# Performance work log

Measured on AMD Instinct MI355X. Metric: run time of the kernel, lower is better.

Reference implementation:

```python
import jax, jax.numpy as jnp
import numpy as np

EPS = 1e-5
SLOPE = 0.01  # torch LeakyReLU default negative slope


def _bn(h, gamma, beta):
    # BatchNorm1d in training mode: biased batch statistics over the batch dim
    mu = jnp.mean(h, axis=0)
    var = jnp.var(h, axis=0)
    return gamma * (h - mu) * jax.lax.rsqrt(var + EPS) + beta


def _leaky(h):
    return jnp.where(h >= 0, h, SLOPE * h)


def _forward(x, adj, w_gc1, b_gc1, w_gc2, b_gc2, w_gc3, b_gc3,
             w_fc0, b_fc0, g_fc0, be_fc0, w_fc1, b_fc1, g_fc1, be_fc1, w_fc2, b_fc2):
    B, S, Fp1 = x.shape
    F = Fp1 - 1
    N = adj.shape[0]
    # --- scatter: build per-sample node features from first S-1 timesteps ---
    sids = x[:, :S - 1, -2].astype(jnp.int32)                                   # [B,S-1]
    feats = jnp.concatenate([x[:, :S - 1, :-2], x[:, :S - 1, -1:]], axis=-1)    # [B,S-1,F]
    X = jnp.zeros((B, N, F), x.dtype).at[jnp.arange(B)[:, None], sids].set(feats)
    # --- symmetric-normalized adjacency with self loops: D^-1/2 (A+I) D^-1/2 ---
    A = adj + jnp.eye(N, dtype=adj.dtype)
    d = jax.lax.rsqrt(jnp.sum(A, axis=1))
    Ahat = d[:, None] * A * d[None, :]                                          # [N,N]
    # --- fc0 branch on last-timestep features ---
    h0 = _leaky(_bn(x[:, -1, :-2] @ w_fc0 + b_fc0, g_fc0, be_fc0))              # [B,FH]
    # --- 3-layer GCN: relu(Ahat @ X @ W + b) ---
    X = jax.nn.relu(jnp.einsum('mn,bnf->bmf', Ahat, X) @ w_gc1 + b_gc1)
    X = jax.nn.relu(jnp.einsum('mn,bnf->bmf', Ahat, X) @ w_gc2 + b_gc2)
    X = jax.nn.relu(jnp.einsum('mn,bnf->bmf', Ahat, X) @ w_gc3 + b_gc3)         # [B,N,GH]
    # --- gather station-specific rows ---
    sid_last = x[:, -1, -2].astype(jnp.int32)                                   # [B]
    g = X[jnp.arange(B), sid_last]                                              # [B,GH]
    # --- fusion MLP head ---
    h = jnp.concatenate([h0, g], axis=1)
    h = _leaky(_bn(h @ w_fc1 + b_fc1, g_fc1, be_fc1))
    return jax.nn.sigmoid(h @ w_fc2 + b_fc2)                                    # [B,1]


def setup_inputs() -> dict:
    B, N, S, F = 128, 2000, 64, 16
    GH, FH = 512, 512
    key = jax.random.key(0)
    ks = jax.random.split(key, 12)
    x = jax.random.normal(ks[0], (B, S, F + 1), dtype=jnp.float32)
    # station-id column (-2): unique ids per sample so scatter writes are unambiguous
    perms = jax.vmap(lambda k: jax.random.permutation(k, N)[:S])(jax.random.split(ks[1], B))  # [B,S]
    x = x.at[:, :, -2].set(perms.astype(jnp.float32))
    # random symmetric 0/1 adjacency, avg degree ~32
    adj = (jax.random.uniform(ks[2], (N, N)) < (32.0 / N)).astype(jnp.float32)
    adj = jnp.maximum(adj, adj.T)

    def lin(k, i, o):
        kw, kb = jax.random.split(k)
        bound = 1.0 / np.sqrt(i)
        w = jax.random.uniform(kw, (i, o), jnp.float32, -bound, bound)
        b = jax.random.uniform(kb, (o,), jnp.float32, -bound, bound)
        return w, b

    w_gc1, b_gc1 = lin(ks[3], F, GH // 2)
    w_gc2, b_gc2 = lin(ks[4], GH // 2, GH // 2)
    w_gc3, b_gc3 = lin(ks[5], GH // 2, GH)
    w_fc0, b_fc0 = lin(ks[6], F - 1, FH)
    w_fc1, b_fc1 = lin(ks[7], GH + FH, FH)
    w_fc2, b_fc2 = lin(ks[8], FH, 1)
    g_fc0 = jnp.ones((FH,), jnp.float32)
    be_fc0 = jnp.zeros((FH,), jnp.float32)
    g_fc1 = jnp.ones((FH,), jnp.float32)
    be_fc1 = jnp.zeros((FH,), jnp.float32)
    return dict(x=x, adj=adj, w_gc1=w_gc1, b_gc1=b_gc1, w_gc2=w_gc2, b_gc2=b_gc2,
                w_gc3=w_gc3, b_gc3=b_gc3, w_fc0=w_fc0, b_fc0=b_fc0, g_fc0=g_fc0, be_fc0=be_fc0,
                w_fc1=w_fc1, b_fc1=b_fc1, g_fc1=g_fc1, be_fc1=be_fc1, w_fc2=w_fc2, b_fc2=b_fc2)


def reference(x, adj, w_gc1, b_gc1, w_gc2, b_gc2, w_gc3, b_gc3, w_fc0, b_fc0, g_fc0, be_fc0,
              w_fc1, b_fc1, g_fc1, be_fc1, w_fc2, b_fc2):
    return _forward(x, adj, w_gc1, b_gc1, w_gc2, b_gc2, w_gc3, b_gc3,
                    w_fc0, b_fc0, g_fc0, be_fc0, w_fc1, b_fc1, g_fc1, be_fc1, w_fc2, b_fc2)
```

## Files before the change

### kernel.cpp

```cpp
#include <hip/hip_runtime.h>
#include <hip/hip_bf16.h>

typedef __hip_bfloat16 bf16;
typedef short s8v __attribute__((ext_vector_type(8)));
typedef float f4v __attribute__((ext_vector_type(4)));
typedef float f2v __attribute__((ext_vector_type(2)));

#define B   128
#define N   2000
#define S   64
#define CAP 128
#define JT  16
#define JG  8
#define XROW 1088

__device__ inline ushort bfb(float v) {
    union { __hip_bfloat16 h; ushort u; } c; c.h = __float2bfloat16(v); return c.u;
}

__global__ __launch_bounds__(256) void k_prep0(const float* __restrict__ adj,
                                               float* __restrict__ d,
                                               const float* __restrict__ w1,
                                               const float* __restrict__ w2,
                                               uint4* __restrict__ wf1,
                                               uint4* __restrict__ wf2) {
    int blk = blockIdx.x;
    if (blk < N) {
        int m = blk;
        const float* row = adj + (size_t)m * N;
        float s = 0.f;
        for (int c = threadIdx.x; c < N; c += 256) s += row[c];
        for (int o = 32; o > 0; o >>= 1) s += __shfl_down(s, o);
        __shared__ float red[4];
        int wave = threadIdx.x >> 6;
        if ((threadIdx.x & 63) == 0) red[wave] = s;
        __syncthreads();
        if (threadIdx.x == 0)
            d[m] = rsqrtf(red[0] + red[1] + red[2] + red[3] + 1.0f);
    } else {
        int blk2 = blk - N;
        if (blk2 < 4) {
            int e = blk2 * 256 + threadIdx.x;
            int ct = e >> 6, l = e & 63;
            int kg = l >> 4, ch = ct * 16 + (l & 15);
            ushort h[8];
#pragma unroll
            for (int j = 0; j < 8; ++j) {
                int f = kg * 8 + j;
                h[j] = (f < 16) ? bfb(w1[f * 256 + ch]) : (ushort)0;
            }
            uint4 r;
            r.x = h[0] | ((uint)h[1] << 16);
            r.y = h[2] | ((uint)h[3] << 16);
            r.z = h[4] | ((uint)h[5] << 16);
            r.w = h[6] | ((uint)h[7] << 16);
            wf1[e] = r;
        } else {
            int e = (blk2 - 4) * 256 + threadIdx.x;
            int l = e & 63;
            int kc = (e >> 6) & 7;
            int nt = e >> 9;
            int col = l & 15, kg = l >> 4;
            ushort h[8];
#pragma unroll
            for (int i = 0; i < 8; ++i) {
                int k = kc * 32 + kg * 8 + i;
                h[i] = bfb(w2[k * 256 + nt * 16 + col]);
            }
            uint4 r;
            r.x = h[0] | ((uint)h[1] << 16);
            r.y = h[2] | ((uint)h[3] << 16);
            r.z = h[4] | ((uint)h[5] << 16);
            r.w = h[6] | ((uint)h[7] << 16);
            wf2[e] = r;
        }
    }
}

__global__ __launch_bounds__(256) void k_prep1(const float* __restrict__ adj,
                                               const float* __restrict__ d,
                                               const float* __restrict__ x,
                                               int* __restrict__ cnt,
                                               int* __restrict__ idx,
                                               float* __restrict__ val,
                                               int* __restrict__ sid,
                                               int* __restrict__ sid_last,
                                               uint4* __restrict__ feA,
                                               const float* __restrict__ w0,
                                               const float* __restrict__ b0,
                                               float* __restrict__ hp0,
                                               float* __restrict__ mu0,
                                               float* __restrict__ rstd0) {
    int blk = blockIdx.x;
    if (blk < 500) {
        int m = blk * 4 + (threadIdx.x >> 6);
        int lane = threadIdx.x & 63;
        const float* row = adj + (size_t)m * N;
        float dm = d[m];
        int base = 0;
        for (int c0 = 0; c0 < N; c0 += 64) {
            int c = c0 + lane;
            float a = 0.f;
            if (c < N) { a = row[c]; if (c == m) a += 1.0f; }
            bool pred = (a != 0.f);
            unsigned long long mask = __ballot(pred);
            int pos = base + __popcll(mask & ((1ull << lane) - 1ull));
            if (pred && pos < CAP) {
                idx[m * CAP + pos] = c;
                val[m * CAP + pos] = dm * d[c] * a;
            }
            base += (int)__popcll(mask);
        }
        if (lane == 0) cnt[m] = base < CAP ? base : CAP;
    } else if (blk < 500 + B) {
        int b = blk - 500, tid = threadIdx.x;
        const float* xb = x + (size_t)b * XROW;
        __shared__ float dss_sh[63];
        __shared__ float fe_sh[64][16];
        if (tid < S - 1) {
            int s_ = (int)xb[tid * 17 + 15];
            sid[b * (S - 1) + tid] = s_;
            dss_sh[tid] = d[s_];
        }
        if (tid == S - 1) sid_last[b] = (int)xb[(S - 1) * 17 + 15];
        if (tid >= 240 && tid < 256) fe_sh[63][tid - 240] = 0.f;
        __syncthreads();
        for (int i = tid; i < (S - 1) * 16; i += 256) {
            int t = i >> 4, f = i & 15;
            fe_sh[t][f] = dss_sh[t] * xb[t * 17 + (f < 15 ? f : 16)];
        }
        __syncthreads();
        if (tid < 128) {
            int kc = tid >> 6, l = tid & 63;
            int f = l & 15, tg = l >> 4;
            ushort h[8];
#pragma unroll
            for (int j = 0; j < 8; ++j)
                h[j] = bfb(fe_sh[kc * 32 + tg * 8 + j][f]);
            uint4 r;
            r.x = h[0] | ((uint)h[1] << 16);
            r.y = h[2] | ((uint)h[3] << 16);
            r.z = h[4] | ((uint)h[5] << 16);
            r.w = h[6] | ((uint)h[7] << 16);
            feA[(b * 2 + kc) * 64 + l] = r;
        }
    } else {
        int tid = threadIdx.x;
        int c = tid >> 7, b = tid & 127;
        int o = (blk - 500 - B) * 2 + c;
        const float* xr = x + (size_t)b * XROW + (S - 1) * 17;
        float acc = b0[o];
#pragma unroll
        for (int f = 0; f < 15; ++f) acc += xr[f] * w0[f * 512 + o];
        hp0[b * 512 + o] = acc;
        float s = acc, s2 = acc * acc;
        for (int off = 32; off > 0; off >>= 1) {
            s += __shfl_down(s, off);
            s2 += __shfl_down(s2, off);
        }
        __shared__ float rs[4], rs2[4];
        int wv = tid >> 6;
        if ((tid & 63) == 0) { rs[wv] = s; rs2[wv] = s2; }
        __syncthreads();
        if ((tid & 127) == 0) {
            float S1 = rs[c * 2] + rs[c * 2 + 1];
            float S2 = rs2[c * 2] + rs2[c * 2 + 1];
            float m = S1 * (1.f / B);
            float var = S2 * (1.f / B) - m * m;
            mu0[o] = m;
            rstd0[o] = rsqrtf(var + 1e-5f);
        }
    }
}

__global__ __launch_bounds__(256) void k_x1(const float* __restrict__ adj,
                                            const float* __restrict__ d,
                                            const int* __restrict__ sid,
                                            const uint4* __restrict__ feA,
                                            const uint4* __restrict__ wfrag,
                                            const float* __restrict__ b1,
                                            unsigned char* __restrict__ X1) {
    __shared__ int sv[64];
    __shared__ float b1s[256];
    __shared__ __align__(16) union SU {
        ushort Ylds[64][40];
        uint   Xs[4][16][68];
    } su;
    int b = blockIdx.y, p0 = blockIdx.x * 64, tid = threadIdx.x;
    b1s[tid] = b1[tid];
    if (tid < 63) sv[tid] = sid[b * 63 + tid];
    if (tid == 63) sv[63] = 0;
    __syncthreads();

    int l = tid & 63, wv = tid >> 6;
    int lm = l & 15, lg = l >> 4;
    int pt = p0 + wv * 16;
    int pcol = pt + lm;
    bool pv = (pcol < N);
    int pc = pv ? pcol : 0;

    s8v a1_0 = *(const s8v*)&feA[(b * 2 + 0) * 64 + l];
    s8v a1_1 = *(const s8v*)&feA[(b * 2 + 1) * 64 + l];

    int ss[16];
#pragma unroll
    for (int q = 0; q < 16; ++q)
        ss[q] = sv[(q >> 3) * 32 + lg * 8 + (q & 7)];
    float av[16];
#pragma unroll
    for (int q = 0; q < 16; ++q)
        av[q] = adj[(size_t)ss[q] * N + pc];
#pragma unroll
    for (int q = 0; q < 16; ++q) {
        av[q] = pv ? av[q] : 0.f;
        if (pcol == ss[q]) av[q] += 1.0f;
    }
    ushort h[16];
#pragma unroll
    for (int q = 0; q < 16; ++q) h[q] = bfb(av[q]);
    s8v b1f, b2f;
    {
        uint4 t0, t1;
        t0.x = h[0] | ((uint)h[1] << 16);  t0.y = h[2] | ((uint)h[3] << 16);
        t0.z = h[4] | ((uint)h[5] << 16);  t0.w = h[6] | ((uint)h[7] << 16);
        t1.x = h[8] | ((uint)h[9] << 16);  t1.y = h[10] | ((uint)h[11] << 16);
        t1.z = h[12] | ((uint)h[13] << 16); t1.w = h[14] | ((uint)h[15] << 16);
        b1f = *(s8v*)&t0; b2f = *(s8v*)&t1;
    }
    f4v D1 = (f4v){0.f, 0.f, 0.f, 0.f};
    D1 = __builtin_amdgcn_mfma_f32_16x16x32_bf16(a1_0, b1f, D1, 0, 0, 0);
    D1 = __builtin_amdgcn_mfma_f32_16x16x32_bf16(a1_1, b2f, D1, 0, 0, 0);
    float dp = d[pc] * (pv ? 1.f : 0.f);
    uint2 pk;
    pk.x = bfb(D1[0] * dp) | ((uint)bfb(D1[1] * dp) << 16);
    pk.y = bfb(D1[2] * dp) | ((uint)bfb(D1[3] * dp) << 16);
    *(uint2*)&su.Ylds[wv * 16 + lm][lg * 4] = pk;
    *(uint2*)&su.Ylds[wv * 16 + lm][16 + lg * 4] = make_uint2(0u, 0u);
    __syncthreads();

    s8v yf = *(const s8v*)&su.Ylds[wv * 16 + lm][lg * 8];
    __syncthreads();
    f4v acc2[16];
#pragma unroll
    for (int ct = 0; ct < 16; ++ct) acc2[ct] = (f4v){0.f, 0.f, 0.f, 0.f};
#pragma unroll
    for (int ct = 0; ct < 16; ++ct) {
        s8v wfv = *(const s8v*)&wfrag[ct * 64 + l];
        acc2[ct] = __builtin_amdgcn_mfma_f32_16x16x32_bf16(wfv, yf, acc2[ct], 0, 0, 0);
    }
#pragma unroll
    for (int ct = 0; ct < 16; ++ct) {
        float4 bz = *(float4*)&b1s[ct * 16 + lg * 4];
        float v0 = acc2[ct][0] + bz.x; v0 = v0 > 0.f ? v0 : 0.f;
        float v1 = acc2[ct][1] + bz.y; v1 = v1 > 0.f ? v1 : 0.f;
        float v2 = acc2[ct][2] + bz.z; v2 = v2 > 0.f ? v2 : 0.f;
        float v3 = acc2[ct][3] + bz.w; v3 = v3 > 0.f ? v3 : 0.f;
        uint pk8 = (uint)__builtin_amdgcn_cvt_pk_fp8_f32(v0, v1, 0, false);
        pk8 = (uint)__builtin_amdgcn_cvt_pk_fp8_f32(v2, v3, (int)pk8, true);
        su.Xs[wv][lm][ct * 4 + lg] = pk8;
    }
    __syncthreads();
    {
        uint4* dstb = (uint4*)((uint*)X1 + ((size_t)b * N + p0 + wv * 16) * 64);
#pragma unroll
        for (int i = 0; i < 4; ++i) {
            int g = l + 64 * i;
            int r = g >> 4, c4 = g & 15;
            if (p0 + wv * 16 + r < N)
                dstb[g] = *(uint4*)&su.Xs[wv][r][c4 * 4];
        }
    }
}

__global__ __launch_bounds__(256) void k_gather(const int* __restrict__ cnt,
                                                const int* __restrict__ idxA,
                                                const float* __restrict__ valA,
                                                const int* __restrict__ sid_last,
                                                const unsigned char* __restrict__ X1,
                                                unsigned char* __restrict__ aggG) {
    __shared__ int   nns[JG];
    __shared__ int   ncn_s[JG];
    __shared__ int   nidx[JG][CAP];
    __shared__ float nval[JG][CAP];
    int b = blockIdx.y, j0 = blockIdx.x * JG, tid = threadIdx.x;
    int m = sid_last[b];
    int cj = cnt[m];
    if (tid < JG) {
        int j = j0 + tid;
        int n = idxA[m * CAP + (j < cj ? j : 0)];
        nns[tid] = n;
        ncn_s[tid] = (j < cj) ? cnt[n] : 0;
    }
    __syncthreads();
    for (int i = tid; i < JG * CAP; i += 256) {
        int jj = i >> 7, k = i & (CAP - 1);
        int n = nns[jj], c = ncn_s[jj];
        nidx[jj][k] = (k < c) ? idxA[n * CAP + k] : 0;
        nval[jj][k] = (k < c) ? valA[n * CAP + k] : 0.f;
    }
    __syncthreads();
    int lane = tid & 63;
    int w = __builtin_amdgcn_readfirstlane(tid >> 6);
    int la = w * 2, lb = la + 1;
    const uint* X1bl = (const uint*)X1 + (size_t)b * N * 64 + lane;
    int cA = ncn_s[la], cB = ncn_s[lb];
    int cmax = cA > cB ? cA : cB;
    float aA0 = 0.f, aA1 = 0.f, aA2 = 0.f, aA3 = 0.f;
    float aB0 = 0.f, aB1 = 0.f, aB2 = 0.f, aB3 = 0.f;
    if (cmax > 0) {
        uint uA0, uA1, uA2, uA3, uB0, uB1, uB2, uB3;
        float vA0, vA1, vA2, vA3, vB0, vB1, vB2, vB3;
        uA0 = X1bl[(size_t)nidx[la][0] * 64]; vA0 = nval[la][0];
        uA1 = X1bl[(size_t)nidx[la][1] * 64]; vA1 = nval[la][1];
        uA2 = X1bl[(size_t)nidx[la][2] * 64]; vA2 = nval[la][2];
        uA3 = X1bl[(size_t)nidx[la][3] * 64]; vA3 = nval[la][3];
        uB0 = X1bl[(size_t)nidx[lb][0] * 64]; vB0 = nval[lb][0];
        uB1 = X1bl[(size_t)nidx[lb][1] * 64]; vB1 = nval[lb][1];
        uB2 = X1bl[(size_t)nidx[lb][2] * 64]; vB2 = nval[lb][2];
        uB3 = X1bl[(size_t)nidx[lb][3] * 64]; vB3 = nval[lb][3];
        int c4 = (cmax + 3) & ~3;
        for (int k = 0; k < c4; k += 4) {
            uint cA0 = uA0, cA1 = uA1, cA2 = uA2, cA3 = uA3;
            uint cB0 = uB0, cB1 = uB1, cB2 = uB2, cB3 = uB3;
            float wA0 = vA0, wA1 = vA1, wA2 = vA2, wA3 = vA3;
            float wB0 = vB0, wB1 = vB1, wB2 = vB2, wB3 = vB3;
            int k4 = k + 4; k4 = k4 < CAP ? k4 : CAP - 1;
            int k5 = k + 5; k5 = k5 < CAP ? k5 : CAP - 1;
            int k6 = k + 6; k6 = k6 < CAP ? k6 : CAP - 1;
            int k7 = k + 7; k7 = k7 < CAP ? k7 : CAP - 1;
            uA0 = X1bl[(size_t)nidx[la][k4] * 64]; vA0 = nval[la][k4];
            uA1 = X1bl[(size_t)nidx[la][k5] * 64]; vA1 = nval[la][k5];
            uA2 = X1bl[(size_t)nidx[la][k6] * 64]; vA2 = nval[la][k6];
            uA3 = X1bl[(size_t)nidx[la][k7] * 64]; vA3 = nval[la][k7];
            uB0 = X1bl[(size_t)nidx[lb][k4] * 64]; vB0 = nval[lb][k4];
            uB1 = X1bl[(size_t)nidx[lb][k5] * 64]; vB1 = nval[lb][k5];
            uB2 = X1bl[(size_t)nidx[lb][k6] * 64]; vB2 = nval[lb][k6];
            uB3 = X1bl[(size_t)nidx[lb][k7] * 64]; vB3 = nval[lb][k7];
            f2v lo, hi;
            lo = __builtin_amdgcn_cvt_pk_f32_fp8((int)cA0, false);
            hi = __builtin_amdgcn_cvt_pk_f32_fp8((int)cA0, true);
            aA0 += wA0 * lo.x; aA1 += wA0 * lo.y; aA2 += wA0 * hi.x; aA3 += wA0 * hi.y;
            lo = __builtin_amdgcn_cvt_pk_f32_fp8((int)cA1, false);
            hi = __builtin_amdgcn_cvt_pk_f32_fp8((int)cA1, true);
            aA0 += wA1 * lo.x; aA1 += wA1 * lo.y; aA2 += wA1 * hi.x; aA3 += wA1 * hi.y;
            lo = __builtin_amdgcn_cvt_pk_f32_fp8((int)cA2, false);
            hi = __builtin_amdgcn_cvt_pk_f32_fp8((int)cA2, true);
            aA0 += wA2 * lo.x; aA1 += wA2 * lo.y; aA2 += wA2 * hi.x; aA3 += wA2 * hi.y;
            lo = __builtin_amdgcn_cvt_pk_f32_fp8((int)cA3, false);
            hi = __builtin_amdgcn_cvt_pk_f32_fp8((int)cA3, true);
            aA0 += wA3 * lo.x; aA1 += wA3 * lo.y; aA2 += wA3 * hi.x; aA3 += wA3 * hi.y;
            lo = __builtin_amdgcn_cvt_pk_f32_fp8((int)cB0, false);
            hi = __builtin_amdgcn_cvt_pk_f32_fp8((int)cB0, true);
            aB0 += wB0 * lo.x; aB1 += wB0 * lo.y; aB2 += wB0 * hi.x; aB3 += wB0 * hi.y;
            lo = __builtin_amdgcn_cvt_pk_f32_fp8((int)cB1, false);
            hi = __builtin_amdgcn_cvt_pk_f32_fp8((int)cB1, true);
            aB0 += wB1 * lo.x; aB1 += wB1 * lo.y; aB2 += wB1 * hi.x; aB3 += wB1 * hi.y;
            lo = __builtin_amdgcn_cvt_pk_f32_fp8((int)cB2, false);
            hi = __builtin_amdgcn_cvt_pk_f32_fp8((int)cB2, true);
            aB0 += wB2 * lo.x; aB1 += wB2 * lo.y; aB2 += wB2 * hi.x; aB3 += wB2 * hi.y;
            lo = __builtin_amdgcn_cvt_pk_f32_fp8((int)cB3, false);
            hi = __builtin_amdgcn_cvt_pk_f32_fp8((int)cB3, true);
            aB0 += wB3 * lo.x; aB1 += wB3 * lo.y; aB2 += wB3 * hi.x; aB3 += wB3 * hi.y;
        }
    }
    uint pkA = (uint)__builtin_amdgcn_cvt_pk_fp8_f32(aA0, aA1, 0, false);
    pkA = (uint)__builtin_amdgcn_cvt_pk_fp8_f32(aA2, aA3, (int)pkA, true);
    uint pkB = (uint)__builtin_amdgcn_cvt_pk_fp8_f32(aB0, aB1, 0, false);
    pkB = (uint)__builtin_amdgcn_cvt_pk_fp8_f32(aB2, aB3, (int)pkB, true);
    uint* ag = (uint*)aggG;
    ag[((size_t)b * CAP + j0 + la) * 64 + lane] = pkA;
    ag[((size_t)b * CAP + j0 + lb) * 64 + lane] = pkB;
}

__global__ __launch_bounds__(256) void k_x2g(const int* __restrict__ cnt,
                                             const int* __restrict__ sid_last,
                                             const float* __restrict__ valA,
                                             const unsigned char* __restrict__ aggG,
                                             const uint4* __restrict__ w2f,
                                             const float* __restrict__ b2,
                                             float* __restrict__ gaggP) {
    __shared__ ushort agg[JT][264];
    __shared__ float vs[JT];
    int b = blockIdx.y, j0 = blockIdx.x * JT, tid = threadIdx.x;
    int m = sid_last[b];
    int cj = cnt[m];
    if (j0 >= cj) return;
    int nj = cj - j0; if (nj > JT) nj = JT;
    if (tid < JT) vs[tid] = (tid < nj) ? valA[m * CAP + j0 + tid] : 0.f;
    {
        const uint* src = (const uint*)aggG + ((size_t)b * CAP + j0) * 64;
        for (int i = tid; i < JT * 64; i += 256) {
            int row = i >> 6, ln = i & 63;
            uint u8 = src[(size_t)row * 64 + ln];
            f2v lo = __builtin_amdgcn_cvt_pk_f32_fp8((int)u8, false);
            f2v hi = __builtin_amdgcn_cvt_pk_f32_fp8((int)u8, true);
            uint2 pk;
            pk.x = bfb(lo.x) | ((uint)bfb(lo.y) << 16);
            pk.y = bfb(hi.x) | ((uint)bfb(hi.y) << 16);
            *(uint2*)&agg[row][ln * 4] = pk;
        }
    }
    __syncthreads();
    int lane = tid & 63;
    int w = __builtin_amdgcn_readfirstlane(tid >> 6);
    int col = lane & 15, rg = lane >> 4;
    s8v af[8];
#pragma unroll
    for (int kc = 0; kc < 8; ++kc)
        af[kc] = *(const s8v*)&agg[col][kc * 32 + rg * 8];
    float* outp = gaggP + ((size_t)b * 8 + blockIdx.x) * 256;
#pragma unroll
    for (int t = 0; t < 4; ++t) {
        int nt = w * 4 + t;
        f4v acc = (f4v){0.f, 0.f, 0.f, 0.f};
#pragma unroll
        for (int kc = 0; kc < 8; ++kc) {
            s8v bf = *(const s8v*)&w2f[(nt * 8 + kc) * 64 + lane];
            acc = __builtin_amdgcn_mfma_f32_16x16x32_bf16(af[kc], bf, acc, 0, 0, 0);
        }
        float bv = b2[nt * 16 + col];
        float p = 0.f;
#pragma unroll
        for (int i = 0; i < 4; ++i) {
            float vv = acc[i] + bv;
            vv = vv > 0.f ? vv : 0.f;
            p += vs[rg * 4 + i] * vv;
        }
        p += __shfl_xor(p, 16);
        p += __shfl_xor(p, 32);
        if (lane < 16) outp[nt * 16 + col] = p;
    }
}

__global__ __launch_bounds__(256) void k_gmm(const int* __restrict__ cnt,
                                             const int* __restrict__ sid_last,
                                             const float* __restrict__ gaggP,
                                             const float* __restrict__ w3,
                                             const float* __restrict__ b3,
                                             float* __restrict__ g) {
    int b = blockIdx.x, ot = blockIdx.y, tid = threadIdx.x;
    __shared__ float h[256];
    {
        int m = sid_last[b];
        int cj = cnt[m];
        int nq = (cj + JT - 1) / JT;
        const float* p = gaggP + (size_t)b * 8 * 256 + tid;
        float s = 0.f;
        for (int q = 0; q < nq; ++q) s += p[q * 256];
        h[tid] = s;
    }
    __syncthreads();
    int q  = tid & 31;
    int kg = tid >> 5;
    const float4* w4 = (const float4*)w3;
    int wq = ot * 32 + q;
    float4 acc = {0.f, 0.f, 0.f, 0.f};
    for (int k = kg * 32; k < kg * 32 + 32; ++k) {
        float hk = h[k];
        float4 w = w4[(size_t)k * 128 + wq];
        acc.x += hk * w.x; acc.y += hk * w.y; acc.z += hk * w.z; acc.w += hk * w.w;
    }
    __shared__ float4 red[8][32];
    red[kg][q] = acc;
    __syncthreads();
    if (tid < 32) {
        float4 s = red[0][tid];
#pragma unroll
        for (int gr = 1; gr < 8; ++gr) {
            float4 r = red[gr][tid];
            s.x += r.x; s.y += r.y; s.z += r.z; s.w += r.w;
        }
        int ob = ot * 128 + tid * 4;
        s.x += b3[ob];     s.x = s.x > 0.f ? s.x : 0.f;
        s.y += b3[ob + 1]; s.y = s.y > 0.f ? s.y : 0.f;
        s.z += b3[ob + 2]; s.z = s.z > 0.f ? s.z : 0.f;
        s.w += b3[ob + 3]; s.w = s.w > 0.f ? s.w : 0.f;
        *(float4*)&g[(size_t)b * 512 + ob] = s;
    }
}

__global__ __launch_bounds__(256) void k_bn1w(const float* __restrict__ h,
                                              float* __restrict__ mu,
                                              float* __restrict__ rstd) {
    int tid = threadIdx.x;
    int o = blockIdx.x * 32 + (tid & 31);
    int bg = tid >> 5;
    float s = 0.f, s2 = 0.f;
    for (int b = bg * 16; b < bg * 16 + 16; ++b) {
        float v = h[b * 512 + o];
        s += v; s2 += v * v;
    }
    __shared__ float rs[8][32], rs2[8][32];
    rs[bg][tid & 31] = s; rs2[bg][tid & 31] = s2;
    __syncthreads();
    if (tid < 32) {
        float S1 = 0.f, S2 = 0.f;
#pragma unroll
        for (int g2 = 0; g2 < 8; ++g2) { S1 += rs[g2][tid]; S2 += rs2[g2][tid]; }
        float m = S1 * (1.f / B);
        float var = S2 * (1.f / B) - m * m;
        mu[blockIdx.x * 32 + tid] = m;
        rstd[blockIdx.x * 32 + tid] = rsqrtf(var + 1e-5f);
    }
}

__global__ __launch_bounds__(256) void k_fc1(const float* __restrict__ hp0,
                                             const float* __restrict__ mu0,
                                             const float* __restrict__ rstd0,
                                             const float* __restrict__ gam,
                                             const float* __restrict__ bet,
                                             const float* __restrict__ gbuf,
                                             const float* __restrict__ w1,
                                             const float* __restrict__ b1,
                                             float* __restrict__ hp1) {
    int b = blockIdx.x, ot = blockIdx.y, tid = threadIdx.x;
    __shared__ float h[1024];
    for (int o = tid; o < 512; o += 256) {
        float v = hp0[b * 512 + o];
        v = gam[o] * (v - mu0[o]) * rstd0[o] + bet[o];
        h[o] = v >= 0.f ? v : 0.01f * v;
        h[512 + o] = gbuf[(size_t)b * 512 + o];
    }
    __syncthreads();
    int q  = tid & 31;
    int kg = tid >> 5;
    const float4* w4 = (const float4*)w1;
    int wq = ot * 32 + q;
    float4 acc = {0.f, 0.f, 0.f, 0.f};
    for (int k = kg * 128; k < kg * 128 + 128; ++k) {
        float hk = h[k];
        float4 w = w4[(size_t)k * 128 + wq];
        acc.x += hk * w.x; acc.y += hk * w.y; acc.z += hk * w.z; acc.w += hk * w.w;
    }
    __shared__ float4 red[8][32];
    red[kg][q] = acc;
    __syncthreads();
    if (tid < 32) {
        float4 s = red[0][tid];
#pragma unroll
        for (int gr = 1; gr < 8; ++gr) {
            float4 r = red[gr][tid];
            s.x += r.x; s.y += r.y; s.z += r.z; s.w += r.w;
        }
        int ob = ot * 128 + tid * 4;
        s.x += b1[ob]; s.y += b1[ob + 1]; s.z += b1[ob + 2]; s.w += b1[ob + 3];
        *(float4*)&hp1[b * 512 + ob] = s;
    }
}

__global__ __launch_bounds__(64) void k_out(const float* __restrict__ hp1,
                                            const float* __restrict__ mu1,
                                            const float* __restrict__ rstd1,
                                            const float* __restrict__ gam,
                                            const float* __restrict__ bet,
                                            const float* __restrict__ w2,
                                            const float* __restrict__ b2,
                                            float* __restrict__ out) {
    int b = blockIdx.x, lane = threadIdx.x;
    float acc = 0.f;
    for (int o = lane; o < 512; o += 64) {
        float v = hp1[b * 512 + o];
        v = gam[o] * (v - mu1[o]) * rstd1[o] + bet[o];
        v = v >= 0.f ? v : 0.01f * v;
        acc += v * w2[o];
    }
    for (int off = 32; off > 0; off >>= 1) acc += __shfl_down(acc, off);
    if (lane == 0) out[b] = 1.f / (1.f + expf(-(acc + b2[0])));
}

static inline size_t align256(size_t x) { return (x + 255) & ~(size_t)255; }

extern "C" void kernel_launch(void* const* d_in, const int* in_sizes, int n_in,
                              void* d_out, int out_size, void* d_ws, size_t ws_size,
                              hipStream_t stream) {
    const float* x     = (const float*)d_in[0];
    const float* adj   = (const float*)d_in[1];
    const float* w_gc1 = (const float*)d_in[2];
    const float* b_gc1 = (const float*)d_in[3];
    const float* w_gc2 = (const float*)d_in[4];
    const float* b_gc2 = (const float*)d_in[5];
    const float* w_gc3 = (const float*)d_in[6];
    const float* b_gc3 = (const float*)d_in[7];
    const float* w_fc0 = (const float*)d_in[8];
    const float* b_fc0 = (const float*)d_in[9];
    const float* g_fc0 = (const float*)d_in[10];
    const float* be_fc0= (const float*)d_in[11];
    const float* w_fc1 = (const float*)d_in[12];
    const float* b_fc1 = (const float*)d_in[13];
    const float* g_fc1 = (const float*)d_in[14];
    const float* be_fc1= (const float*)d_in[15];
    const float* w_fc2 = (const float*)d_in[16];
    const float* b_fc2 = (const float*)d_in[17];

    char* wsp = (char*)d_ws;
    size_t off = 0;
    auto alloc = [&](size_t bytes) { void* p = wsp + off; off = align256(off + bytes); return p; };
    float* d_deg   = (float*)alloc((size_t)N * 4);
    int*   sid     = (int*)  alloc((size_t)B * 63 * 4);
    int*   sidl    = (int*)  alloc((size_t)B * 4);
    uint4* feA     = (uint4*)alloc((size_t)B * 2 * 64 * 16);
    uint4* wfrag   = (uint4*)alloc((size_t)1024 * 16);
    uint4* w2frag  = (uint4*)alloc((size_t)8192 * 16);
    int*   csr_cnt = (int*)  alloc((size_t)N * 4);
    int*   csr_idx = (int*)  alloc((size_t)N * CAP * 4);
    float* csr_val = (float*)alloc((size_t)N * CAP * 4);
    unsigned char* X1   = (unsigned char*)alloc((size_t)B * N * 256);
    unsigned char* aggG = (unsigned char*)alloc((size_t)B * CAP * 256);
    float* gaggP   = (float*)alloc((size_t)B * 8 * 256 * 4);
    float* gbuf    = (float*)alloc((size_t)B * 512 * 4);
    float* hp0     = (float*)alloc((size_t)B * 512 * 4);
    float* mu0     = (float*)alloc(512 * 4);
    float* rstd0   = (float*)alloc(512 * 4);
    float* hp1     = (float*)alloc((size_t)B * 512 * 4);
    float* mu1     = (float*)alloc(512 * 4);
    float* rstd1   = (float*)alloc(512 * 4);

    k_prep0 <<<N + 36, 256, 0, stream>>>(adj, d_deg, w_gc1, w_gc2, wfrag, w2frag);
    k_prep1 <<<500 + B + 256, 256, 0, stream>>>(adj, d_deg, x, csr_cnt, csr_idx, csr_val,
                                                sid, sidl, feA, w_fc0, b_fc0, hp0, mu0, rstd0);
    k_x1    <<<dim3(32, B), 256, 0, stream>>>(adj, d_deg, sid, feA, wfrag, b_gc1, X1);
    k_gather<<<dim3(CAP / JG, B), 256, 0, stream>>>(csr_cnt, csr_idx, csr_val, sidl, X1, aggG);
    k_x2g   <<<dim3(CAP / JT, B), 256, 0, stream>>>(csr_cnt, sidl, csr_val, aggG, w2frag, b_gc2, gaggP);
    k_gmm   <<<dim3(B, 4), 256, 0, stream>>>(csr_cnt, sidl, gaggP, w_gc3, b_gc3, gbuf);
    k_fc1   <<<dim3(B, 4), 256, 0, stream>>>(hp0, mu0, rstd0, g_fc0, be_fc0, gbuf, w_fc1, b_fc1, hp1);
    k_bn1w  <<<16, 256, 0, stream>>>(hp1, mu1, rstd1);
    k_out   <<<B, 64, 0, stream>>>(hp1, mu1, rstd1, g_fc1, be_fc1, w_fc2, b_fc2, (float*)d_out);
}
```

Baseline: 119.2 us.

## Replace per-sample fc1 GEMV with bf16 MFMA GEMM over batch

Converts the fc1 weight into bf16 MFMA fragments during prep and replaces the per-sample fp32 GEMV (which reread the whole weight for every sample) with a single batched MFMA GEMM. The BN+LeakyReLU of the fc0 branch and the GCN output are written as bf16 activations by k_gmm via an extra block column. This cuts redundant weight traffic, at the cost of bf16 precision in fc1, a per-call weight conversion, and a GEMM launched with only 8 blocks.

```diff
diff --git a/kernel.cpp b/kernel.cpp
--- a/kernel.cpp
+++ b/kernel.cpp
@@ -22,8 +22,10 @@
                                                float* __restrict__ d,
                                                const float* __restrict__ w1,
                                                const float* __restrict__ w2,
+                                               const float* __restrict__ wfc1,
                                                uint4* __restrict__ wf1,
-                                               uint4* __restrict__ wf2) {
+                                               uint4* __restrict__ wf2,
+                                               uint4* __restrict__ wf3) {
     int blk = blockIdx.x;
     if (blk < N) {
         int m = blk;
@@ -37,7 +39,7 @@
         __syncthreads();
         if (threadIdx.x == 0)
             d[m] = rsqrtf(red[0] + red[1] + red[2] + red[3] + 1.0f);
-    } else {
+    } else if (blk < N + 36) {
         int blk2 = blk - N;
         if (blk2 < 4) {
             int e = blk2 * 256 + threadIdx.x;
@@ -74,6 +76,24 @@
             r.w = h[6] | ((uint)h[7] << 16);
             wf2[e] = r;
         }
+    } else {
+        int e = (blk - N - 36) * 256 + threadIdx.x;
+        int l = e & 63;
+        int kc = (e >> 6) & 31;
+        int nt = e >> 11;
+        int col = l & 15, kg = l >> 4;
+        ushort h[8];
+#pragma unroll
+        for (int i = 0; i < 8; ++i) {
+            int k = kc * 32 + kg * 8 + i;
+            h[i] = bfb(wfc1[(size_t)k * 512 + nt * 16 + col]);
+        }
+        uint4 r;
+        r.x = h[0] | ((uint)h[1] << 16);
+        r.y = h[2] | ((uint)h[3] << 16);
+        r.z = h[4] | ((uint)h[5] << 16);
+        r.w = h[6] | ((uint)h[7] << 16);
+        wf3[e] = r;
     }
 }
 
@@ -437,8 +457,22 @@
                                              const float* __restrict__ gaggP,
                                              const float* __restrict__ w3,
                                              const float* __restrict__ b3,
-                                             float* __restrict__ g) {
+                                             const float* __restrict__ hp0,
+                                             const float* __restrict__ mu0,
+                                             const float* __restrict__ rstd0,
+                                             const float* __restrict__ gam,
+                                             const float* __restrict__ bet,
+                                             ushort* __restrict__ hbf) {
     int b = blockIdx.x, ot = blockIdx.y, tid = threadIdx.x;
+    if (ot == 4) {
+        for (int o = tid; o < 512; o += 256) {
+            float v = hp0[b * 512 + o];
+            v = gam[o] * (v - mu0[o]) * rstd0[o] + bet[o];
+            v = v >= 0.f ? v : 0.01f * v;
+            hbf[(size_t)b * 1024 + o] = bfb(v);
+        }
+        return;
+    }
     __shared__ float h[256];
     {
         int m = sid_last[b];
@@ -475,7 +509,43 @@
         s.y += b3[ob + 1]; s.y = s.y > 0.f ? s.y : 0.f;
         s.z += b3[ob + 2]; s.z = s.z > 0.f ? s.z : 0.f;
         s.w += b3[ob + 3]; s.w = s.w > 0.f ? s.w : 0.f;
-        *(float4*)&g[(size_t)b * 512 + ob] = s;
+        uint2 pk;
+        pk.x = bfb(s.x) | ((uint)bfb(s.y) << 16);
+        pk.y = bfb(s.z) | ((uint)bfb(s.w) << 16);
+        *(uint2*)&hbf[(size_t)b * 1024 + 512 + ob] = pk;
+    }
+}
+
+__global__ __launch_bounds__(256) void k_fc1mm(const ushort* __restrict__ hbf,
+                                               const uint4* __restrict__ w3f,
+                                               const float* __restrict__ b1,
+                                               float* __restrict__ hp1) {
+    int tid = threadIdx.x;
+    int l = tid & 63;
+    int w = __builtin_amdgcn_readfirstlane(tid >> 6);
+    int ct_g = blockIdx.x * 4 + w;
+    int lm = l & 15, lg = l >> 4;
+    f4v acc[8];
+#pragma unroll
+    for (int rt = 0; rt < 8; ++rt) acc[rt] = (f4v){0.f, 0.f, 0.f, 0.f};
+    for (int kc = 0; kc < 32; ++kc) {
+        s8v bf = *(const s8v*)&w3f[(ct_g * 32 + kc) * 64 + l];
+#pragma unroll
+        for (int rt = 0; rt < 8; ++rt) {
+            const ushort* ap = hbf + (size_t)(rt * 16 + lm) * 1024 + kc * 32 + lg * 8;
+            s8v af = *(const s8v*)ap;
+            acc[rt] = __builtin_amdgcn_mfma_f32_16x16x32_bf16(af, bf, acc[rt], 0, 0, 0);
+        }
+    }
+    int n = ct_g * 16 + lm;
+    float bv = b1[n];
+#pragma unroll
+    for (int rt = 0; rt < 8; ++rt) {
+#pragma unroll
+        for (int i = 0; i < 4; ++i) {
+            int mrow = rt * 16 + lg * 4 + i;
+            hp1[(size_t)mrow * 512 + n] = acc[rt][i] + bv;
+        }
     }
 }
 
@@ -501,50 +571,6 @@
         float var = S2 * (1.f / B) - m * m;
         mu[blockIdx.x * 32 + tid] = m;
         rstd[blockIdx.x * 32 + tid] = rsqrtf(var + 1e-5f);
-    }
-}
-
-__global__ __launch_bounds__(256) void k_fc1(const float* __restrict__ hp0,
-                                             const float* __restrict__ mu0,
-                                             const float* __restrict__ rstd0,
-                                             const float* __restrict__ gam,
-                                             const float* __restrict__ bet,
-                                             const float* __restrict__ gbuf,
-                                             const float* __restrict__ w1,
-                                             const float* __restrict__ b1,
-                                             float* __restrict__ hp1) {
-    int b = blockIdx.x, ot = blockIdx.y, tid = threadIdx.x;
-    __shared__ float h[1024];
-    for (int o = tid; o < 512; o += 256) {
-        float v = hp0[b * 512 + o];
-        v = gam[o] * (v - mu0[o]) * rstd0[o] + bet[o];
-        h[o] = v >= 0.f ? v : 0.01f * v;
-        h[512 + o] = gbuf[(size_t)b * 512 + o];
-    }
-    __syncthreads();
-    int q  = tid & 31;
-    int kg = tid >> 5;
-    const float4* w4 = (const float4*)w1;
-    int wq = ot * 32 + q;
-    float4 acc = {0.f, 0.f, 0.f, 0.f};
-    for (int k = kg * 128; k < kg * 128 + 128; ++k) {
-        float hk = h[k];
-        float4 w = w4[(size_t)k * 128 + wq];
-        acc.x += hk * w.x; acc.y += hk * w.y; acc.z += hk * w.z; acc.w += hk * w.w;
-    }
-    __shared__ float4 red[8][32];
-    red[kg][q] = acc;
-    __syncthreads();
-    if (tid < 32) {
-        float4 s = red[0][tid];
-#pragma unroll
-        for (int gr = 1; gr < 8; ++gr) {
-            float4 r = red[gr][tid];
-            s.x += r.x; s.y += r.y; s.z += r.z; s.w += r.w;
-        }
-        int ob = ot * 128 + tid * 4;
-        s.x += b1[ob]; s.y += b1[ob + 1]; s.z += b1[ob + 2]; s.w += b1[ob + 3];
-        *(float4*)&hp1[b * 512 + ob] = s;
     }
 }
 
@@ -601,13 +627,14 @@
     uint4* feA     = (uint4*)alloc((size_t)B * 2 * 64 * 16);
     uint4* wfrag   = (uint4*)alloc((size_t)1024 * 16);
     uint4* w2frag  = (uint4*)alloc((size_t)8192 * 16);
+    uint4* w3frag  = (uint4*)alloc((size_t)65536 * 16);
     int*   csr_cnt = (int*)  alloc((size_t)N * 4);
     int*   csr_idx = (int*)  alloc((size_t)N * CAP * 4);
     float* csr_val = (float*)alloc((size_t)N * CAP * 4);
     unsigned char* X1   = (unsigned char*)alloc((size_t)B * N * 256);
     unsigned char* aggG = (unsigned char*)alloc((size_t)B * CAP * 256);
     float* gaggP   = (float*)alloc((size_t)B * 8 * 256 * 4);
-    float* gbuf    = (float*)alloc((size_t)B * 512 * 4);
+    ushort* hbf    = (ushort*)alloc((size_t)B * 1024 * 2);
     float* hp0     = (float*)alloc((size_t)B * 512 * 4);
     float* mu0     = (float*)alloc(512 * 4);
     float* rstd0   = (float*)alloc(512 * 4);
@@ -615,14 +642,16 @@
     float* mu1     = (float*)alloc(512 * 4);
     float* rstd1   = (float*)alloc(512 * 4);
 
-    k_prep0 <<<N + 36, 256, 0, stream>>>(adj, d_deg, w_gc1, w_gc2, wfrag, w2frag);
+    k_prep0 <<<N + 36 + 256, 256, 0, stream>>>(adj, d_deg, w_gc1, w_gc2, w_fc1,
+                                               wfrag, w2frag, w3frag);
     k_prep1 <<<500 + B + 256, 256, 0, stream>>>(adj, d_deg, x, csr_cnt, csr_idx, csr_val,
                                                 sid, sidl, feA, w_fc0, b_fc0, hp0, mu0, rstd0);
     k_x1    <<<dim3(32, B), 256, 0, stream>>>(adj, d_deg, sid, feA, wfrag, b_gc1, X1);
     k_gather<<<dim3(CAP / JG, B), 256, 0, stream>>>(csr_cnt, csr_idx, csr_val, sidl, X1, aggG);
     k_x2g   <<<dim3(CAP / JT, B), 256, 0, stream>>>(csr_cnt, sidl, csr_val, aggG, w2frag, b_gc2, gaggP);
-    k_gmm   <<<dim3(B, 4), 256, 0, stream>>>(csr_cnt, sidl, gaggP, w_gc3, b_gc3, gbuf);
-    k_fc1   <<<dim3(B, 4), 256, 0, stream>>>(hp0, mu0, rstd0, g_fc0, be_fc0, gbuf, w_fc1, b_fc1, hp1);
+    k_gmm   <<<dim3(B, 5), 256, 0, stream>>>(csr_cnt, sidl, gaggP, w_gc3, b_gc3,
+                                             hp0, mu0, rstd0, g_fc0, be_fc0, hbf);
+    k_fc1mm <<<8, 256, 0, stream>>>(hbf, w3frag, b_fc1, hp1);
     k_bn1w  <<<16, 256, 0, stream>>>(hp1, mu1, rstd1);
     k_out   <<<B, 64, 0, stream>>>(hp1, mu1, rstd1, g_fc1, be_fc1, w_fc2, b_fc2, (float*)d_out);
 }
```

New measurement: 140.7 us. 18.0% more time.
